# Performance work log

Measured on AMD Instinct MI355X. Metric: run time of the kernel, lower is better.

## Reference

```python
import jax, jax.numpy as jnp
import numpy as np


def _cdist(a, b, p):
    # a: [B, N, D], b: [B, M, D] -> [B, N, M] pairwise Lp distance
    diff = jnp.abs(a[:, :, None, :] - b[:, None, :, :])  # [B, N, M, D]
    if p == 1:
        return jnp.sum(diff, axis=-1)
    return jnp.sum(diff ** p, axis=-1) ** (1.0 / p)


def setup_inputs() -> dict:
    key = jax.random.key(0)
    k1, k2, k3 = jax.random.split(key, 3)
    B, P, D = 32, 2048, 2
    pred = jax.random.normal(k1, (B, P, D), dtype=jnp.float32)
    gt = jax.random.normal(k2, (B, P, D), dtype=jnp.float32)
    gt_valid = jax.random.normal(k3, (B, P, D), dtype=jnp.float32)
    return {"pred": pred, "gt": gt, "gt_valid": gt_valid, "loss_type": 1}


def reference(pred, gt, gt_valid, loss_type):
    # matrix = cdist(pred, gt): [B, Np, Ng]; torch.min(dim=1) reduces over Np
    m1 = _cdist(pred, gt, loss_type)
    pred2gt_min = jnp.min(m1, axis=1)  # [B, Ng]
    # matrix = cdist(gt_valid, pred): [B, Ngv, Np]; min over dim=1 (Ngv)
    m2 = _cdist(gt_valid, pred, loss_type)
    gt2pred_min = jnp.min(m2, axis=1)  # [B, Np]
    return jnp.mean(jnp.stack([jnp.mean(pred2gt_min), jnp.mean(gt2pred_min)]))
```

## Files before the change

kernel.cpp:

```cpp
#include <hip/hip_runtime.h>


typedef float v2f __attribute__((ext_vector_type(2)));

#define BB 32
#define NN 2048
#define TPB 512
#define WAVES 8
#define TGT 128
#define CH (NN / WAVES)
#define NTILES (NN / TGT)
#define NBLK (2 * BB * NTILES)

__global__ __launch_bounds__(TPB) void chamfer_l1_part(
    const float* __restrict__ pred,
    const float* __restrict__ gt,
    const float* __restrict__ gt_valid,
    float* __restrict__ bsum)
{
    const int bid  = blockIdx.x;
    const int dir  = bid >> 9;
    const int rem  = bid & 511;
    const int b    = rem >> 4;
    const int tile = rem & (NTILES - 1);
    const int lane = threadIdx.x & 63;
    const int wid  = threadIdx.x >> 6;

    const float* __restrict__ tgt = (dir == 0 ? gt   : pred)     + (size_t)b * NN * 2;
    const float* __restrict__ src = (dir == 0 ? pred : gt_valid) + (size_t)b * NN * 2;

    __shared__ v2f lds_src[NN];
    {
        const float4* gsrc = reinterpret_cast<const float4*>(src);
        float4*       lsrc = reinterpret_cast<float4*>(lds_src);
        lsrc[threadIdx.x]       = gsrc[threadIdx.x];
        lsrc[threadIdx.x + TPB] = gsrc[threadIdx.x + TPB];
    }

    const int j0 = tile * TGT + lane;
    v2f pA, pB;
    {
        float2 tA = reinterpret_cast<const float2*>(tgt)[j0];
        float2 tB = reinterpret_cast<const float2*>(tgt)[j0 + 64];
        pA = (v2f){tA.x, tA.y};
        pB = (v2f){tB.x, tB.y};
    }
    __syncthreads();

    const v2f* __restrict__ ls = lds_src + wid * CH;
    float a0 = 1e30f, a1 = 1e30f, a2 = 1e30f, a3 = 1e30f;
    float b0 = 1e30f, b1 = 1e30f, b2 = 1e30f, b3 = 1e30f;
    #pragma unroll 4
    for (int s = 0; s < CH; s += 8) {
        v2f q0 = ls[s+0], q1 = ls[s+1], q2 = ls[s+2], q3 = ls[s+3];
        v2f q4 = ls[s+4], q5 = ls[s+5], q6 = ls[s+6], q7 = ls[s+7];

        v2f dA0 = q0 - pA, dA1 = q1 - pA, dA2 = q2 - pA, dA3 = q3 - pA;
        v2f dA4 = q4 - pA, dA5 = q5 - pA, dA6 = q6 - pA, dA7 = q7 - pA;
        v2f dB0 = q0 - pB, dB1 = q1 - pB, dB2 = q2 - pB, dB3 = q3 - pB;
        v2f dB4 = q4 - pB, dB5 = q5 - pB, dB6 = q6 - pB, dB7 = q7 - pB;

        float sA0 = fabsf(dA0.x) + fabsf(dA0.y);
        float sA1 = fabsf(dA1.x) + fabsf(dA1.y);
        float sA2 = fabsf(dA2.x) + fabsf(dA2.y);
        float sA3 = fabsf(dA3.x) + fabsf(dA3.y);
        float sA4 = fabsf(dA4.x) + fabsf(dA4.y);
        float sA5 = fabsf(dA5.x) + fabsf(dA5.y);
        float sA6 = fabsf(dA6.x) + fabsf(dA6.y);
        float sA7 = fabsf(dA7.x) + fabsf(dA7.y);
        float sB0 = fabsf(dB0.x) + fabsf(dB0.y);
        float sB1 = fabsf(dB1.x) + fabsf(dB1.y);
        float sB2 = fabsf(dB2.x) + fabsf(dB2.y);
        float sB3 = fabsf(dB3.x) + fabsf(dB3.y);
        float sB4 = fabsf(dB4.x) + fabsf(dB4.y);
        float sB5 = fabsf(dB5.x) + fabsf(dB5.y);
        float sB6 = fabsf(dB6.x) + fabsf(dB6.y);
        float sB7 = fabsf(dB7.x) + fabsf(dB7.y);

        a0 = fminf(a0, fminf(sA0, sA1));
        a1 = fminf(a1, fminf(sA2, sA3));
        a2 = fminf(a2, fminf(sA4, sA5));
        a3 = fminf(a3, fminf(sA6, sA7));
        b0 = fminf(b0, fminf(sB0, sB1));
        b1 = fminf(b1, fminf(sB2, sB3));
        b2 = fminf(b2, fminf(sB4, sB5));
        b3 = fminf(b3, fminf(sB6, sB7));
    }
    const float mA = fminf(fminf(a0, a1), fminf(a2, a3));
    const float mB = fminf(fminf(b0, b1), fminf(b2, b3));

    __shared__ float part[WAVES][TGT];
    part[wid][lane]      = mA;
    part[wid][64 + lane] = mB;
    __syncthreads();

    __shared__ float wpart[2];
    if (threadIdx.x < 128) {
        const int t = threadIdx.x;
        float mm = part[0][t];
        #pragma unroll
        for (int w = 1; w < WAVES; ++w) mm = fminf(mm, part[w][t]);
        for (int off = 32; off > 0; off >>= 1)
            mm += __shfl_down(mm, off, 64);
        if ((t & 63) == 0) wpart[t >> 6] = mm;
    }
    __syncthreads();
    if (threadIdx.x == 0) bsum[bid] = wpart[0] + wpart[1];
}

__global__ __launch_bounds__(256) void chamfer_l1_reduce(
    const float* __restrict__ bsum,
    float* __restrict__ out)
{
    const int t = threadIdx.x;
    float4 v = reinterpret_cast<const float4*>(bsum)[t];
    float s = (v.x + v.y) + (v.z + v.w);
    for (int off = 32; off > 0; off >>= 1)
        s += __shfl_down(s, off, 64);
    __shared__ float w[4];
    if ((t & 63) == 0) w[t >> 6] = s;
    __syncthreads();
    if (t == 0)
        out[0] = (w[0] + w[1] + w[2] + w[3]) * (1.0f / (2.0f * BB * NN));
}

extern "C" void kernel_launch(void* const* d_in, const int* in_sizes, int n_in,
                              void* d_out, int out_size, void* d_ws, size_t ws_size,
                              hipStream_t stream) {
    const float* pred     = (const float*)d_in[0];
    const float* gt       = (const float*)d_in[1];
    const float* gt_valid = (const float*)d_in[2];
    float* out  = (float*)d_out;
    float* bsum = (float*)d_ws;

    chamfer_l1_part<<<NBLK, TPB, 0, stream>>>(pred, gt, gt_valid, bsum);
    chamfer_l1_reduce<<<1, 256, 0, stream>>>(bsum, out);
}
```

Before: 80.31 us.

## Double per-thread target count and use 128-bit LDS loads in chamfer kernel

Each block now covers 256 target points instead of 128, with each thread holding four targets in registers, so every source point read from LDS is reused across four distance computations. The per-block source staging and LDS traffic are amortized over twice the work, and LDS reads are widened to float4. This halves the grid to 512 blocks, which lowers parallelism and adds register pressure, and the reduction kernel is adjusted to read 512 partial sums.

```diff
diff --git a/kernel.cpp b/kernel.cpp
--- a/kernel.cpp
+++ b/kernel.cpp
@@ -7,7 +7,7 @@
 #define NN 2048
 #define TPB 512
 #define WAVES 8
-#define TGT 128
+#define TGT 256
 #define CH (NN / WAVES)
 #define NTILES (NN / TGT)
 #define NBLK (2 * BB * NTILES)
@@ -19,9 +19,9 @@
     float* __restrict__ bsum)
 {
     const int bid  = blockIdx.x;
-    const int dir  = bid >> 9;
-    const int rem  = bid & 511;
-    const int b    = rem >> 4;
+    const int dir  = bid >> 8;
+    const int rem  = bid & 255;
+    const int b    = rem >> 3;
     const int tile = rem & (NTILES - 1);
     const int lane = threadIdx.x & 63;
     const int wid  = threadIdx.x >> 6;
@@ -38,64 +38,69 @@
     }
 
     const int j0 = tile * TGT + lane;
-    v2f pA, pB;
+    v2f p0, p1, p2, p3;
     {
-        float2 tA = reinterpret_cast<const float2*>(tgt)[j0];
-        float2 tB = reinterpret_cast<const float2*>(tgt)[j0 + 64];
-        pA = (v2f){tA.x, tA.y};
-        pB = (v2f){tB.x, tB.y};
+        float2 t0 = reinterpret_cast<const float2*>(tgt)[j0];
+        float2 t1 = reinterpret_cast<const float2*>(tgt)[j0 + 64];
+        float2 t2 = reinterpret_cast<const float2*>(tgt)[j0 + 128];
+        float2 t3 = reinterpret_cast<const float2*>(tgt)[j0 + 192];
+        p0 = (v2f){t0.x, t0.y};
+        p1 = (v2f){t1.x, t1.y};
+        p2 = (v2f){t2.x, t2.y};
+        p3 = (v2f){t3.x, t3.y};
     }
     __syncthreads();
 
-    const v2f* __restrict__ ls = lds_src + wid * CH;
-    float a0 = 1e30f, a1 = 1e30f, a2 = 1e30f, a3 = 1e30f;
-    float b0 = 1e30f, b1 = 1e30f, b2 = 1e30f, b3 = 1e30f;
-    #pragma unroll 4
-    for (int s = 0; s < CH; s += 8) {
-        v2f q0 = ls[s+0], q1 = ls[s+1], q2 = ls[s+2], q3 = ls[s+3];
-        v2f q4 = ls[s+4], q5 = ls[s+5], q6 = ls[s+6], q7 = ls[s+7];
+    const float4* __restrict__ ls4 =
+        reinterpret_cast<const float4*>(lds_src + (size_t)wid * CH);
 
-        v2f dA0 = q0 - pA, dA1 = q1 - pA, dA2 = q2 - pA, dA3 = q3 - pA;
-        v2f dA4 = q4 - pA, dA5 = q5 - pA, dA6 = q6 - pA, dA7 = q7 - pA;
-        v2f dB0 = q0 - pB, dB1 = q1 - pB, dB2 = q2 - pB, dB3 = q3 - pB;
-        v2f dB4 = q4 - pB, dB5 = q5 - pB, dB6 = q6 - pB, dB7 = q7 - pB;
+    float c00 = 1e30f, c01 = 1e30f, c10 = 1e30f, c11 = 1e30f;
+    float c20 = 1e30f, c21 = 1e30f, c30 = 1e30f, c31 = 1e30f;
 
-        float sA0 = fabsf(dA0.x) + fabsf(dA0.y);
-        float sA1 = fabsf(dA1.x) + fabsf(dA1.y);
-        float sA2 = fabsf(dA2.x) + fabsf(dA2.y);
-        float sA3 = fabsf(dA3.x) + fabsf(dA3.y);
-        float sA4 = fabsf(dA4.x) + fabsf(dA4.y);
-        float sA5 = fabsf(dA5.x) + fabsf(dA5.y);
-        float sA6 = fabsf(dA6.x) + fabsf(dA6.y);
-        float sA7 = fabsf(dA7.x) + fabsf(dA7.y);
-        float sB0 = fabsf(dB0.x) + fabsf(dB0.y);
-        float sB1 = fabsf(dB1.x) + fabsf(dB1.y);
-        float sB2 = fabsf(dB2.x) + fabsf(dB2.y);
-        float sB3 = fabsf(dB3.x) + fabsf(dB3.y);
-        float sB4 = fabsf(dB4.x) + fabsf(dB4.y);
-        float sB5 = fabsf(dB5.x) + fabsf(dB5.y);
-        float sB6 = fabsf(dB6.x) + fabsf(dB6.y);
-        float sB7 = fabsf(dB7.x) + fabsf(dB7.y);
+    #pragma unroll 2
+    for (int s = 0; s < CH / 2; s += 4) {
+        float4 f0 = ls4[s + 0];
+        float4 f1 = ls4[s + 1];
+        float4 f2 = ls4[s + 2];
+        float4 f3 = ls4[s + 3];
+        v2f q0 = (v2f){f0.x, f0.y}, q1 = (v2f){f0.z, f0.w};
+        v2f q2 = (v2f){f1.x, f1.y}, q3 = (v2f){f1.z, f1.w};
+        v2f q4 = (v2f){f2.x, f2.y}, q5 = (v2f){f2.z, f2.w};
+        v2f q6 = (v2f){f3.x, f3.y}, q7 = (v2f){f3.z, f3.w};
 
-        a0 = fminf(a0, fminf(sA0, sA1));
-        a1 = fminf(a1, fminf(sA2, sA3));
-        a2 = fminf(a2, fminf(sA4, sA5));
-        a3 = fminf(a3, fminf(sA6, sA7));
-        b0 = fminf(b0, fminf(sB0, sB1));
-        b1 = fminf(b1, fminf(sB2, sB3));
-        b2 = fminf(b2, fminf(sB4, sB5));
-        b3 = fminf(b3, fminf(sB6, sB7));
+        #define L1S(q, p) (fabsf((q).x - (p).x) + fabsf((q).y - (p).y))
+        c00 = fminf(c00, fminf(L1S(q0,p0), L1S(q1,p0)));
+        c00 = fminf(c00, fminf(L1S(q2,p0), L1S(q3,p0)));
+        c01 = fminf(c01, fminf(L1S(q4,p0), L1S(q5,p0)));
+        c01 = fminf(c01, fminf(L1S(q6,p0), L1S(q7,p0)));
+        c10 = fminf(c10, fminf(L1S(q0,p1), L1S(q1,p1)));
+        c10 = fminf(c10, fminf(L1S(q2,p1), L1S(q3,p1)));
+        c11 = fminf(c11, fminf(L1S(q4,p1), L1S(q5,p1)));
+        c11 = fminf(c11, fminf(L1S(q6,p1), L1S(q7,p1)));
+        c20 = fminf(c20, fminf(L1S(q0,p2), L1S(q1,p2)));
+        c20 = fminf(c20, fminf(L1S(q2,p2), L1S(q3,p2)));
+        c21 = fminf(c21, fminf(L1S(q4,p2), L1S(q5,p2)));
+        c21 = fminf(c21, fminf(L1S(q6,p2), L1S(q7,p2)));
+        c30 = fminf(c30, fminf(L1S(q0,p3), L1S(q1,p3)));
+        c30 = fminf(c30, fminf(L1S(q2,p3), L1S(q3,p3)));
+        c31 = fminf(c31, fminf(L1S(q4,p3), L1S(q5,p3)));
+        c31 = fminf(c31, fminf(L1S(q6,p3), L1S(q7,p3)));
+        #undef L1S
     }
-    const float mA = fminf(fminf(a0, a1), fminf(a2, a3));
-    const float mB = fminf(fminf(b0, b1), fminf(b2, b3));
+    const float m0 = fminf(c00, c01);
+    const float m1 = fminf(c10, c11);
+    const float m2 = fminf(c20, c21);
+    const float m3 = fminf(c30, c31);
 
     __shared__ float part[WAVES][TGT];
-    part[wid][lane]      = mA;
-    part[wid][64 + lane] = mB;
+    part[wid][lane]       = m0;
+    part[wid][lane + 64]  = m1;
+    part[wid][lane + 128] = m2;
+    part[wid][lane + 192] = m3;
     __syncthreads();
 
-    __shared__ float wpart[2];
-    if (threadIdx.x < 128) {
+    __shared__ float wpart[4];
+    if (threadIdx.x < TGT) {
         const int t = threadIdx.x;
         float mm = part[0][t];
         #pragma unroll
@@ -105,7 +110,8 @@
         if ((t & 63) == 0) wpart[t >> 6] = mm;
     }
     __syncthreads();
-    if (threadIdx.x == 0) bsum[bid] = wpart[0] + wpart[1];
+    if (threadIdx.x == 0)
+        bsum[bid] = (wpart[0] + wpart[1]) + (wpart[2] + wpart[3]);
 }
 
 __global__ __launch_bounds__(256) void chamfer_l1_reduce(
@@ -113,8 +119,8 @@
     float* __restrict__ out)
 {
     const int t = threadIdx.x;
-    float4 v = reinterpret_cast<const float4*>(bsum)[t];
-    float s = (v.x + v.y) + (v.z + v.w);
+    float2 v = reinterpret_cast<const float2*>(bsum)[t];
+    float s = v.x + v.y;
     for (int off = 32; off > 0; off >>= 1)
         s += __shfl_down(s, off, 64);
     __shared__ float w[4];
```

New measurement: 82.08 us. 1.02x slower.
